# Kernel optimization log

Hardware: AMD Instinct MI355X
Metric: run time of the kernel (lower is better)

Reference implementation:

```python
import jax, jax.numpy as jnp
import numpy as np

SCALE = 4.0  # InputEmbedding scale
D = 16       # coordinate dim (InputEmbedding input_dim)


def _p(k, shape, s=0.05):
    return jax.random.normal(k, shape, dtype=jnp.float32) * s


def setup_inputs() -> dict:
    key = jax.random.key(0)
    ks = jax.random.split(key, 20)
    T, N, E, H = 8, 2048, 256, 768
    return {
        "observed": jax.random.normal(ks[0], (T, N, D), dtype=jnp.float32),
        "emb_W": _p(ks[1], (E, D)), "emb_b": _p(ks[2], (E,)),
        "e1_Wih": _p(ks[3], (3 * H, E)), "e1_Whh": _p(ks[4], (3 * H, H)),
        "e1_bih": _p(ks[5], (3 * H,)), "e1_bhh": _p(ks[6], (3 * H,)),
        "e2_Wih": _p(ks[7], (3 * H, E + H)), "e2_Whh": _p(ks[8], (3 * H, H)),
        "e2_bih": _p(ks[9], (3 * H,)), "e2_bhh": _p(ks[10], (3 * H,)),
        "dec_Wih": _p(ks[11], (3 * H, E)), "dec_Whh": _p(ks[12], (3 * H, H)),
        "dec_bih": _p(ks[13], (3 * H,)), "dec_bhh": _p(ks[14], (3 * H,)),
        "h2n_W": _p(ks[15], (5, H)), "h2n_b": _p(ks[16], (5,)),
        "mix_W": _p(ks[17], (D, 5)), "mix_b": _p(ks[18], (D,)),
        "n_predict": 12,
    }


def _gru(x, h, Wih, Whh, bih, bhh):
    # torch.nn.GRUCell math
    gi = x @ Wih.T + bih          # [N, 3H]
    gh = h @ Whh.T + bhh          # [N, 3H]
    ir, iz, in_ = jnp.split(gi, 3, axis=-1)
    hr, hz, hn = jnp.split(gh, 3, axis=-1)
    r = jax.nn.sigmoid(ir + hr)
    z = jax.nn.sigmoid(iz + hz)
    n = jnp.tanh(in_ + r * hn)
    return (1.0 - z) * n + z * h


def reference(observed, emb_W, emb_b,
              e1_Wih, e1_Whh, e1_bih, e1_bhh,
              e2_Wih, e2_Whh, e2_bih, e2_bhh,
              dec_Wih, dec_Whh, dec_bih, dec_bhh,
              h2n_W, h2n_b, mix_W, mix_b, n_predict):
    T, N, _ = observed.shape
    H = e1_Whh.shape[1]
    embed = lambda v: (SCALE * v) @ emb_W.T + emb_b   # InputEmbedding
    h0 = jnp.zeros((N, H), observed.dtype)

    # --- backward (inverse-time) encoder1 pass ---
    inv = observed[::-1]
    vel_b = inv[:-1] - inv[1:]          # obs2 - obs1 on reversed sequence, [T-1, N, D]
    def step1(h, v):
        return _gru(embed(v), h, e1_Wih, e1_Whh, e1_bih, e1_bhh), None
    h_inv, _ = jax.lax.scan(step1, h0, vel_b)
    # NOTE: original mutates the python hidden_state list in place, so every
    # h_invs entry aliases the FINAL encoder1 state -> h_inv is constant over t.

    # --- forward encoder2 pass (input = [embed(vel), h_inv]) ---
    vel_f = observed[1:] - observed[:-1]   # [T-1, N, D]
    def step2(h, v):
        x = jnp.concatenate([embed(v), h_inv], axis=1)
        return _gru(x, h, e2_Wih, e2_Whh, e2_bih, e2_bhh), None
    h, _ = jax.lax.scan(step2, h0, vel_f)

    def h2n(hs):
        # Hidden2Normal: linear then constrain sigmas / correlation
        n = hs @ h2n_W.T + h2n_b
        return jnp.concatenate(
            [n[:, :2], 0.01 + 0.2 * jax.nn.softplus(n[:, 2:4]), 0.7 * jnp.tanh(n[:, 4:5])],
            axis=1)

    def dec_step(h, obs1, obs2):
        h = _gru(embed(obs2 - obs1), h, dec_Wih, dec_Whh, dec_bih, dec_bhh)
        normal = h2n(h)                                   # [N, 5]
        pos = obs2 + jax.nn.relu(normal @ mix_W.T + mix_b)  # mix: Linear(5 -> 16)
        return h, normal, pos

    # decoder step i=0: (observed[-2], observed[-1]); i=1: (observed[-1], positions[-1].detach())
    h, n0, p0 = dec_step(h, observed[-2], observed[-1])
    h, n1, p1 = dec_step(h, observed[-1], jax.lax.stop_gradient(p0))

    def scan_step(carry, _):
        h, pm2, pm1 = carry
        h, n, p = dec_step(h, jax.lax.stop_gradient(pm2), jax.lax.stop_gradient(pm1))
        return (h, pm1, p), (n, p)
    _, (ns, ps) = jax.lax.scan(scan_step, (h, p0, p1), None, length=n_predict - 2)

    rel_pred_scene = jnp.concatenate([jnp.stack([n0, n1]), ns], axis=0)  # [n_predict, N, 5]
    pred_scene = jnp.concatenate([jnp.stack([p0, p1]), ps], axis=0)      # [n_predict, N, 16]
    return rel_pred_scene, pred_scene
```

## Files before the change

kernel.cpp:

```cpp
#include <hip/hip_runtime.h>
#include <hip/hip_bf16.h>
#include <math.h>

#define H 768
#define NB 2048
#define DD 16

typedef __attribute__((ext_vector_type(8))) short bf16x8;
typedef __attribute__((ext_vector_type(4))) float f32x4;

__device__ __forceinline__ void gload_lds16(const void* g, void* lds) {
  __builtin_amdgcn_global_load_lds((const __attribute__((address_space(1))) void*)g,
                                   (__attribute__((address_space(3))) void*)lds, 16, 0, 0);
}
__device__ __forceinline__ float b2f(short s) {
  union { unsigned int u; float f; } c;
  c.u = ((unsigned int)(unsigned short)s) << 16;
  return c.f;
}
__device__ __forceinline__ short f2bs(float f) {
  __hip_bfloat16 h = __float2bfloat16(f);
  return *(short*)&h;
}

__global__ void k_m1(const float* __restrict__ e1W, const float* __restrict__ e2W,
                     const float* __restrict__ dW, const float* __restrict__ embW,
                     float* __restrict__ M1) {
  int idx = blockIdx.x * 256 + threadIdx.x;
  if (idx >= 3 * 2304 * 16) return;
  int d = idx & 15, g = (idx >> 4) % 2304, s = idx / (2304 * 16);
  const float* W = s == 0 ? e1W : s == 1 ? e2W : dW;
  int ld = s == 1 ? 1024 : 256;
  float sum = 0.f;
  for (int e = 0; e < 256; ++e) sum += W[(size_t)g * ld + e] * embW[e * 16 + d];
  M1[idx] = 4.0f * sum;
}

__global__ void k_biasP(const float* __restrict__ e1W, const float* __restrict__ e2W,
                        const float* __restrict__ dW, const float* __restrict__ embB,
                        const float* b1i, const float* b1h, const float* b2i, const float* b2h,
                        const float* b3i, const float* b3h, float* __restrict__ out) {
  int idx = blockIdx.x * 256 + threadIdx.x;
  if (idx >= 3 * 3072) return;
  int c = idx % 3072, s = idx / 3072;
  int f = (c >> 4) & 3, u = (c >> 6) * 16 + (c & 15);
  const float* W = s == 0 ? e1W : s == 1 ? e2W : dW;
  int ld = s == 1 ? 1024 : 256;
  const float* bi = s == 0 ? b1i : s == 1 ? b2i : b3i;
  const float* bh = s == 0 ? b1h : s == 1 ? b2h : b3h;
  float v;
  if (f == 3) {
    v = bh[1536 + u];
  } else {
    int g = (f < 2 ? f * 768 : 1536) + u;
    float acc = bi[g] + (f < 2 ? bh[g] : 0.f);
    for (int e = 0; e < 256; ++e) acc += W[(size_t)g * ld + e] * embB[e];
    v = acc;
  }
  out[idx] = v;
}

__global__ void k_packB3(const float* __restrict__ W1, const float* __restrict__ W2,
                         const float* __restrict__ W3, const float* __restrict__ M1all,
                         __hip_bfloat16* __restrict__ B1, __hip_bfloat16* __restrict__ B2,
                         __hip_bfloat16* __restrict__ B3) {
  int idx = blockIdx.x * 256 + threadIdx.x;
  if (idx >= 3072 * 800) return;
  int s = blockIdx.y;
  const float* Whh = s == 0 ? W1 : s == 1 ? W2 : W3;
  const float* M1s = M1all + (size_t)s * 2304 * 16;
  __hip_bfloat16* Bp = s == 0 ? B1 : s == 1 ? B2 : B3;
  int k = idx % 800, c = idx / 800;
  int f = (c >> 4) & 3, u = (c >> 6) * 16 + (c & 15);
  float v = 0.f;
  if (k < 768) {
    if (f == 0) v = Whh[(size_t)u * 768 + k];
    else if (f == 1) v = Whh[(size_t)(768 + u) * 768 + k];
    else if (f == 3) v = Whh[(size_t)(1536 + u) * 768 + k];
  } else if (k < 784) {
    if (f < 3) v = M1s[(size_t)(f * 768 + u) * 16 + (k - 768)];
  }
  Bp[idx] = __float2bfloat16(v);
}

__global__ void k_packB2g(const float* __restrict__ e2W, __hip_bfloat16* __restrict__ B2g) {
  int idx = blockIdx.x * 256 + threadIdx.x;
  if (idx >= 3072 * 768) return;
  int k = idx % 768, c = idx / 768;
  int f = (c >> 4) & 3, u = (c >> 6) * 16 + (c & 15);
  float v = (f < 3) ? e2W[(size_t)(f * 768 + u) * 1024 + 256 + k] : 0.f;
  B2g[idx] = __float2bfloat16(v);
}

__global__ void k_vel(const float* __restrict__ obs, __hip_bfloat16* __restrict__ velall) {
  int idx = blockIdx.x * 256 + threadIdx.x;
  if (idx >= 7 * 2048 * 32) return;
  int d = idx & 31, n = (idx >> 5) & 2047, s = idx >> 16;
  float v = 0.f;
  if (d < 16)
    v = obs[((size_t)(s + 1) * NB + n) * DD + d] - obs[((size_t)s * NB + n) * DD + d];
  velall[idx] = __float2bfloat16(v);
}

__global__ __launch_bounds__(256) void k_plain(
    const __hip_bfloat16* __restrict__ A, const __hip_bfloat16* __restrict__ B,
    __hip_bfloat16* __restrict__ C, int ldc) {
  __shared__ __align__(16) __hip_bfloat16 Asm[128 * 32];
  __shared__ __align__(16) __hip_bfloat16 Bsm[128 * 32];
  const int tid = threadIdx.x;
  const int w = tid >> 6, l = tid & 63;
  const int bm = blockIdx.y, bn = blockIdx.x;
  const int wm = w >> 1, wn = w & 1;
  const int lr = l & 15, lk = l >> 4;
  const int ks = (((tid & 3) ^ ((tid >> 3) & 3)) << 3);
  const int lks = ((lk ^ ((lr >> 1) & 3)) << 3);
  f32x4 acc[4][4];
#pragma unroll
  for (int m = 0; m < 4; ++m)
#pragma unroll
    for (int n = 0; n < 4; ++n) acc[m][n] = (f32x4){0.f, 0.f, 0.f, 0.f};
  const int rowA = bm * 128, rowB = bn * 128;
  const int rA = tid >> 2;
  for (int kb = 0; kb < H; kb += 32) {
#pragma unroll
    for (int i = 0; i < 2; ++i) {
      int r = i * 64 + rA;
      gload_lds16(A + (size_t)(rowA + r) * H + kb + ks, (char*)Asm + i * 4096 + w * 1024);
      gload_lds16(B + (size_t)(rowB + r) * H + kb + ks, (char*)Bsm + i * 4096 + w * 1024);
    }
    __syncthreads();
    bf16x8 af[4], bfr[4];
#pragma unroll
    for (int m = 0; m < 4; ++m)
      af[m] = *(const bf16x8*)(Asm + (wm * 64 + m * 16 + lr) * 32 + lks);
#pragma unroll
    for (int n = 0; n < 4; ++n)
      bfr[n] = *(const bf16x8*)(Bsm + (wn * 64 + n * 16 + lr) * 32 + lks);
#pragma unroll
    for (int m = 0; m < 4; ++m)
#pragma unroll
      for (int n = 0; n < 4; ++n)
        acc[m][n] = __builtin_amdgcn_mfma_f32_16x16x32_bf16(af[m], bfr[n], acc[m][n], 0, 0, 0);
    __syncthreads();
  }
#pragma unroll
  for (int m = 0; m < 4; ++m)
#pragma unroll
    for (int n = 0; n < 4; ++n) {
      int col = bn * 128 + wn * 64 + n * 16 + lr;
#pragma unroll
      for (int r4 = 0; r4 < 4; ++r4) {
        int row = rowA + wm * 64 + m * 16 + lk * 4 + r4;
        C[(size_t)row * ldc + col] = __float2bfloat16(acc[m][n][r4]);
      }
    }
}

__global__ __launch_bounds__(256) void k_step(
    const __hip_bfloat16* __restrict__ hin,
    const __hip_bfloat16* __restrict__ vel,
    const __hip_bfloat16* __restrict__ Bp,
    const float* __restrict__ bias,
    const __hip_bfloat16* __restrict__ g2a,
    __hip_bfloat16* __restrict__ hout) {
  __shared__ __align__(16) char lds[49152];
  const int tid = threadIdx.x;
  const int w = tid >> 6, l = tid & 63;
  const int nt = blockIdx.x, bm = blockIdx.y;
  const int rowA = bm * 128, colB = nt * 64;
  const int lr = l & 15, lk = l >> 4;
  const int wbase = w * 1024;
  const int rA = tid >> 2;
  const int ce = (((tid & 3) ^ ((tid >> 3) & 3)) << 3);
  const int lks = ((lk ^ ((lr >> 1) & 3)) << 3);

  auto STAGE = [&](int buf, int kb) {
#pragma unroll
    for (int i_ = 0; i_ < 2; ++i_) {
      int r_ = i_ * 64 + rA;
      const __hip_bfloat16* s_ = (kb < 768)
          ? hin + (size_t)(rowA + r_) * H + kb + ce
          : vel + (size_t)(rowA + r_) * 32 + ce;
      gload_lds16(s_, lds + buf * 12288 + i_ * 4096 + wbase);
    }
    gload_lds16(Bp + (size_t)(colB + rA) * 800 + kb + ce, lds + buf * 12288 + 8192 + wbase);
  };

  f32x4 acc[2][4];
#pragma unroll
  for (int m = 0; m < 2; ++m)
#pragma unroll
    for (int n = 0; n < 4; ++n) acc[m][n] = (f32x4){0.f, 0.f, 0.f, 0.f};

  STAGE(0, 0);
  STAGE(1, 32);
  STAGE(2, 64);

#pragma unroll
  for (int ki = 0; ki < 25; ++ki) {
    if (ki < 23)      asm volatile("s_waitcnt vmcnt(6)" ::: "memory");
    else if (ki == 23) asm volatile("s_waitcnt vmcnt(3)" ::: "memory");
    else               asm volatile("s_waitcnt vmcnt(0)" ::: "memory");
    __builtin_amdgcn_sched_barrier(0);
    __builtin_amdgcn_s_barrier();
    __builtin_amdgcn_sched_barrier(0);
    if (ki < 22) STAGE((ki + 3) & 3, (ki + 3) * 32);
    const char* cur = lds + (ki & 3) * 12288;
    const __hip_bfloat16* Ab = (const __hip_bfloat16*)cur;
    const __hip_bfloat16* Bb = (const __hip_bfloat16*)(cur + 8192);
    bf16x8 a0 = *(const bf16x8*)(Ab + (w * 32 + lr) * 32 + lks);
    bf16x8 a1 = *(const bf16x8*)(Ab + (w * 32 + 16 + lr) * 32 + lks);
    bf16x8 b0 = *(const bf16x8*)(Bb + lr * 32 + lks);
    bf16x8 b1 = *(const bf16x8*)(Bb + (16 + lr) * 32 + lks);
    const bool last = (ki == 24);
    bf16x8 b2 = *(const bf16x8*)(Bb + ((last ? 32 : 48) + lr) * 32 + lks);
    __builtin_amdgcn_s_setprio(1);
    acc[0][0] = __builtin_amdgcn_mfma_f32_16x16x32_bf16(a0, b0, acc[0][0], 0, 0, 0);
    acc[1][0] = __builtin_amdgcn_mfma_f32_16x16x32_bf16(a1, b0, acc[1][0], 0, 0, 0);
    acc[0][1] = __builtin_amdgcn_mfma_f32_16x16x32_bf16(a0, b1, acc[0][1], 0, 0, 0);
    acc[1][1] = __builtin_amdgcn_mfma_f32_16x16x32_bf16(a1, b1, acc[1][1], 0, 0, 0);
    if (last) {
      acc[0][2] = __builtin_amdgcn_mfma_f32_16x16x32_bf16(a0, b2, acc[0][2], 0, 0, 0);
      acc[1][2] = __builtin_amdgcn_mfma_f32_16x16x32_bf16(a1, b2, acc[1][2], 0, 0, 0);
    } else {
      acc[0][3] = __builtin_amdgcn_mfma_f32_16x16x32_bf16(a0, b2, acc[0][3], 0, 0, 0);
      acc[1][3] = __builtin_amdgcn_mfma_f32_16x16x32_bf16(a1, b2, acc[1][3], 0, 0, 0);
    }
    __builtin_amdgcn_s_setprio(0);
  }

  __syncthreads();
  short* T = (short*)lds;
  const float* bp = bias + nt * 64;
#pragma unroll
  for (int n = 0; n < 4; ++n) {
    float bv = bp[n * 16 + lr];
#pragma unroll
    for (int m = 0; m < 2; ++m) {
      int rbase = w * 32 + m * 16 + lk * 4;
#pragma unroll
      for (int r4 = 0; r4 < 4; ++r4)
        T[(rbase + r4) * 72 + n * 16 + lr] = f2bs(acc[m][n][r4] + bv);
    }
  }
  __syncthreads();

  const int row = tid >> 1;
  const int ub = (tid & 1) * 8;
  const size_t grow = (size_t)(rowA + row);
  const short* Tp = T + row * 72;
  bf16x8 Lr = *(const bf16x8*)(Tp + ub);
  bf16x8 Lz = *(const bf16x8*)(Tp + 16 + ub);
  bf16x8 Li = *(const bf16x8*)(Tp + 32 + ub);
  bf16x8 Lh = *(const bf16x8*)(Tp + 48 + ub);
  bf16x8 h8 = *(const bf16x8*)(hin + grow * H + nt * 16 + ub);
  bf16x8 gr, gz, gi_;
  if (g2a) {
    const __hip_bfloat16* gp = g2a + grow * 3072 + nt * 64;
    gr  = *(const bf16x8*)(gp + ub);
    gz  = *(const bf16x8*)(gp + 16 + ub);
    gi_ = *(const bf16x8*)(gp + 32 + ub);
  }
  union { bf16x8 v; short s[8]; } ob;
#pragma unroll
  for (int e = 0; e < 8; ++e) {
    float xr = b2f(Lr[e]), xz = b2f(Lz[e]), xi = b2f(Li[e]), xh = b2f(Lh[e]);
    if (g2a) { xr += b2f(gr[e]); xz += b2f(gz[e]); xi += b2f(gi_[e]); }
    float r = 1.f / (1.f + expf(-xr));
    float z = 1.f / (1.f + expf(-xz));
    float nn = tanhf(xi + r * xh);
    float hv = (1.f - z) * nn + z * b2f(h8[e]);
    ob.s[e] = f2bs(hv);
  }
  *(bf16x8*)(hout + grow * H + nt * 16 + ub) = ob.v;
}

__global__ void k_head(const __hip_bfloat16* __restrict__ h, const float* __restrict__ obs2,
                       const float* __restrict__ h2n_W, const float* __restrict__ h2n_b,
                       const float* __restrict__ mix_W, const float* __restrict__ mix_b,
                       float* __restrict__ rel_out, float* __restrict__ pos_out,
                       __hip_bfloat16* __restrict__ velout) {
  int wv = threadIdx.x >> 6, lane = threadIdx.x & 63;
  int row = blockIdx.x * 4 + wv;
  float s0 = 0.f, s1 = 0.f, s2 = 0.f, s3 = 0.f, s4 = 0.f;
  for (int k = lane; k < H; k += 64) {
    float hv = b2f(((const short*)h)[(size_t)row * H + k]);
    s0 += hv * h2n_W[k];
    s1 += hv * h2n_W[H + k];
    s2 += hv * h2n_W[2 * H + k];
    s3 += hv * h2n_W[3 * H + k];
    s4 += hv * h2n_W[4 * H + k];
  }
#pragma unroll
  for (int off = 32; off; off >>= 1) {
    s0 += __shfl_down(s0, off);
    s1 += __shfl_down(s1, off);
    s2 += __shfl_down(s2, off);
    s3 += __shfl_down(s3, off);
    s4 += __shfl_down(s4, off);
  }
  s0 = __shfl(s0, 0); s1 = __shfl(s1, 0); s2 = __shfl(s2, 0);
  s3 = __shfl(s3, 0); s4 = __shfl(s4, 0);
  float n0 = s0 + h2n_b[0], n1 = s1 + h2n_b[1];
  float x2 = s2 + h2n_b[2], x3 = s3 + h2n_b[3], x4 = s4 + h2n_b[4];
  float n2 = 0.01f + 0.2f * (x2 > 0.f ? x2 + log1pf(expf(-x2)) : log1pf(expf(x2)));
  float n3 = 0.01f + 0.2f * (x3 > 0.f ? x3 + log1pf(expf(-x3)) : log1pf(expf(x3)));
  float n4 = 0.7f * tanhf(x4);
  float rl = 0.f;
  if (lane < DD) {
    float a = mix_b[lane] + n0 * mix_W[lane * 5 + 0] + n1 * mix_W[lane * 5 + 1] +
              n2 * mix_W[lane * 5 + 2] + n3 * mix_W[lane * 5 + 3] + n4 * mix_W[lane * 5 + 4];
    rl = a > 0.f ? a : 0.f;
    pos_out[(size_t)row * DD + lane] = obs2[(size_t)row * DD + lane] + rl;
  }
  if (lane < 32)
    velout[(size_t)row * 32 + lane] = __float2bfloat16(lane < DD ? rl : 0.f);
  if (lane == 0) {
    rel_out[(size_t)row * 5 + 0] = n0;
    rel_out[(size_t)row * 5 + 1] = n1;
    rel_out[(size_t)row * 5 + 2] = n2;
    rel_out[(size_t)row * 5 + 3] = n3;
    rel_out[(size_t)row * 5 + 4] = n4;
  }
}

extern "C" void kernel_launch(void* const* d_in, const int* in_sizes, int n_in,
                              void* d_out, int out_size, void* d_ws, size_t ws_size,
                              hipStream_t stream) {
  (void)in_sizes; (void)n_in; (void)out_size; (void)ws_size;
  const float* observed = (const float*)d_in[0];
  const float* emb_W   = (const float*)d_in[1];
  const float* emb_b   = (const float*)d_in[2];
  const float* e1_Wih  = (const float*)d_in[3];
  const float* e1_Whh  = (const float*)d_in[4];
  const float* e1_bih  = (const float*)d_in[5];
  const float* e1_bhh  = (const float*)d_in[6];
  const float* e2_Wih  = (const float*)d_in[7];
  const float* e2_Whh  = (const float*)d_in[8];
  const float* e2_bih  = (const float*)d_in[9];
  const float* e2_bhh  = (const float*)d_in[10];
  const float* dec_Wih = (const float*)d_in[11];
  const float* dec_Whh = (const float*)d_in[12];
  const float* dec_bih = (const float*)d_in[13];
  const float* dec_bhh = (const float*)d_in[14];
  const float* h2n_W   = (const float*)d_in[15];
  const float* h2n_b   = (const float*)d_in[16];
  const float* mix_W   = (const float*)d_in[17];
  const float* mix_b   = (const float*)d_in[18];

  char* p = (char*)d_ws;
  auto alloc = [&](size_t bytes) { char* r = p; p += (bytes + 255) & ~(size_t)255; return r; };

  __hip_bfloat16* hz     = (__hip_bfloat16*)alloc((size_t)NB * H * 2);
  __hip_bfloat16* hp0    = (__hip_bfloat16*)alloc((size_t)NB * H * 2);
  __hip_bfloat16* hp1    = (__hip_bfloat16*)alloc((size_t)NB * H * 2);
  __hip_bfloat16* velall = (__hip_bfloat16*)alloc((size_t)7 * NB * 32 * 2);
  __hip_bfloat16* dvel   = (__hip_bfloat16*)alloc((size_t)NB * 32 * 2);
  __hip_bfloat16* Bp1    = (__hip_bfloat16*)alloc((size_t)3072 * 800 * 2);
  __hip_bfloat16* Bp2    = (__hip_bfloat16*)alloc((size_t)3072 * 800 * 2);
  __hip_bfloat16* Bp3    = (__hip_bfloat16*)alloc((size_t)3072 * 800 * 2);
  __hip_bfloat16* B2g    = (__hip_bfloat16*)alloc((size_t)3072 * 768 * 2);
  __hip_bfloat16* g2add  = (__hip_bfloat16*)alloc((size_t)NB * 3072 * 2);
  float*          M1     = (float*)alloc((size_t)3 * 2304 * 16 * 4);
  float*          biasP  = (float*)alloc((size_t)3 * 3072 * 4);

  hipMemsetAsync(hz, 0, (size_t)NB * H * 2, stream);
  k_m1<<<(3 * 2304 * 16 + 255) / 256, 256, 0, stream>>>(e1_Wih, e2_Wih, dec_Wih, emb_W, M1);
  k_biasP<<<(3 * 3072 + 255) / 256, 256, 0, stream>>>(e1_Wih, e2_Wih, dec_Wih, emb_b,
                                                      e1_bih, e1_bhh, e2_bih, e2_bhh,
                                                      dec_bih, dec_bhh, biasP);
  k_packB3<<<dim3((3072 * 800 + 255) / 256, 3), 256, 0, stream>>>(e1_Whh, e2_Whh, dec_Whh,
                                                                  M1, Bp1, Bp2, Bp3);
  k_packB2g<<<(3072 * 768 + 255) / 256, 256, 0, stream>>>(e2_Wih, B2g);
  k_vel<<<(7 * NB * 32 + 255) / 256, 256, 0, stream>>>(observed, velall);

  dim3 gs(48, 16);
  const __hip_bfloat16* src;
  __hip_bfloat16* dst = hp0;

  src = hz;
  for (int t = 0; t < 7; ++t) {
    k_step<<<gs, 256, 0, stream>>>(src, velall + (size_t)(6 - t) * NB * 32, Bp1, biasP,
                                   nullptr, dst);
    src = dst;
    dst = (dst == hp0) ? hp1 : hp0;
  }
  k_plain<<<dim3(24, 16), 256, 0, stream>>>(src, B2g, g2add, 3072);

  src = hz;
  for (int t = 0; t < 7; ++t) {
    k_step<<<gs, 256, 0, stream>>>(src, velall + (size_t)t * NB * 32, Bp2, biasP + 3072,
                                   g2add, dst);
    src = dst;
    dst = (dst == hp0) ? hp1 : hp0;
  }

  float* rel  = (float*)d_out;
  float* pred = (float*)d_out + (size_t)12 * NB * 5;
  for (int k = 0; k < 12; ++k) {
    const __hip_bfloat16* vk = (k == 0) ? velall + (size_t)6 * NB * 32 : dvel;
    k_step<<<gs, 256, 0, stream>>>(src, vk, Bp3, biasP + 2 * 3072, nullptr, dst);
    const float* o2 = (k == 0) ? observed + (size_t)7 * NB * DD
                               : pred + (size_t)(k - 1) * NB * DD;
    k_head<<<NB / 4, 256, 0, stream>>>(dst, o2, h2n_W, h2n_b, mix_W, mix_b,
                                       rel + (size_t)k * NB * 5, pred + (size_t)k * NB * DD,
                                       dvel);
    src = dst;
    dst = (dst == hp0) ? hp1 : hp0;
  }
}
```

Before: 773.3 us.

## Halve step-kernel M tile, use 2x2 warp grid, skip zero-state GEMM

The recurrent step kernel moves from 128-row tiles to 64-row tiles and splits its four waves into a 2x2 layout over M and N. The grid doubles to 48x32 and the LDS ring grows to five stages with a four-deep prefetch, with launch bounds asking for more resident blocks. The first step of each encoder, where the hidden state is zero, now runs only the velocity K-slice, which drops the hidden-state GEMM work and the zero-buffer memset. In exchange each block reuses fewer loaded weights, and B tiles are reloaded across twice as many row blocks.

```diff
diff --git a/kernel.cpp b/kernel.cpp
--- a/kernel.cpp
+++ b/kernel.cpp
@@ -7,6 +7,7 @@
 #define DD 16
 
 typedef __attribute__((ext_vector_type(8))) short bf16x8;
+typedef __attribute__((ext_vector_type(4))) short bf16x4;
 typedef __attribute__((ext_vector_type(4))) float f32x4;
 
 __device__ __forceinline__ void gload_lds16(const void* g, void* lds) {
@@ -156,123 +157,126 @@
     }
 }
 
-__global__ __launch_bounds__(256) void k_step(
+__global__ __launch_bounds__(256, 4) void k_step(
     const __hip_bfloat16* __restrict__ hin,
     const __hip_bfloat16* __restrict__ vel,
     const __hip_bfloat16* __restrict__ Bp,
     const float* __restrict__ bias,
     const __hip_bfloat16* __restrict__ g2a,
     __hip_bfloat16* __restrict__ hout) {
-  __shared__ __align__(16) char lds[49152];
+  __shared__ __align__(16) char lds[40960];
   const int tid = threadIdx.x;
   const int w = tid >> 6, l = tid & 63;
   const int nt = blockIdx.x, bm = blockIdx.y;
-  const int rowA = bm * 128, colB = nt * 64;
+  const int rowA = bm * 64, colB = nt * 64;
   const int lr = l & 15, lk = l >> 4;
-  const int wbase = w * 1024;
-  const int rA = tid >> 2;
+  const int wm = w >> 1, wn = w & 1;
+  const int rS = tid >> 2;
   const int ce = (((tid & 3) ^ ((tid >> 3) & 3)) << 3);
   const int lks = ((lk ^ ((lr >> 1) & 3)) << 3);
+  const int wbase = w * 1024;
 
   auto STAGE = [&](int buf, int kb) {
-#pragma unroll
-    for (int i_ = 0; i_ < 2; ++i_) {
-      int r_ = i_ * 64 + rA;
-      const __hip_bfloat16* s_ = (kb < 768)
-          ? hin + (size_t)(rowA + r_) * H + kb + ce
-          : vel + (size_t)(rowA + r_) * 32 + ce;
-      gload_lds16(s_, lds + buf * 12288 + i_ * 4096 + wbase);
+    const __hip_bfloat16* s_ = (kb < 768)
+        ? hin + (size_t)(rowA + rS) * H + kb + ce
+        : vel + (size_t)(rowA + rS) * 32 + ce;
+    gload_lds16(s_, lds + buf * 8192 + wbase);
+    gload_lds16(Bp + (size_t)(colB + rS) * 800 + kb + ce, lds + buf * 8192 + 4096 + wbase);
+  };
+
+  f32x4 acc[2][2];
+#pragma unroll
+  for (int m = 0; m < 2; ++m)
+#pragma unroll
+    for (int n = 0; n < 2; ++n) acc[m][n] = (f32x4){0.f, 0.f, 0.f, 0.f};
+
+  if (hin) {
+    STAGE(0, 0); STAGE(1, 32); STAGE(2, 64); STAGE(3, 96);
+#pragma unroll
+    for (int ki = 0; ki < 25; ++ki) {
+      if (ki < 22)       asm volatile("s_waitcnt vmcnt(6)" ::: "memory");
+      else if (ki == 22) asm volatile("s_waitcnt vmcnt(4)" ::: "memory");
+      else if (ki == 23) asm volatile("s_waitcnt vmcnt(2)" ::: "memory");
+      else               asm volatile("s_waitcnt vmcnt(0)" ::: "memory");
+      __builtin_amdgcn_sched_barrier(0);
+      __builtin_amdgcn_s_barrier();
+      __builtin_amdgcn_sched_barrier(0);
+      if (ki < 21) STAGE((ki + 4) % 5, (ki + 4) * 32);
+      const char* cur = lds + (ki % 5) * 8192;
+      const __hip_bfloat16* Ab = (const __hip_bfloat16*)cur;
+      const __hip_bfloat16* Bb = (const __hip_bfloat16*)(cur + 4096);
+      bf16x8 a0 = *(const bf16x8*)(Ab + (wm * 32 + lr) * 32 + lks);
+      bf16x8 a1 = *(const bf16x8*)(Ab + (wm * 32 + 16 + lr) * 32 + lks);
+      bf16x8 b0 = *(const bf16x8*)(Bb + (wn * 32 + lr) * 32 + lks);
+      bf16x8 b1 = *(const bf16x8*)(Bb + (wn * 32 + 16 + lr) * 32 + lks);
+      __builtin_amdgcn_s_setprio(1);
+      acc[0][0] = __builtin_amdgcn_mfma_f32_16x16x32_bf16(a0, b0, acc[0][0], 0, 0, 0);
+      acc[1][0] = __builtin_amdgcn_mfma_f32_16x16x32_bf16(a1, b0, acc[1][0], 0, 0, 0);
+      acc[0][1] = __builtin_amdgcn_mfma_f32_16x16x32_bf16(a0, b1, acc[0][1], 0, 0, 0);
+      acc[1][1] = __builtin_amdgcn_mfma_f32_16x16x32_bf16(a1, b1, acc[1][1], 0, 0, 0);
+      __builtin_amdgcn_s_setprio(0);
     }
-    gload_lds16(Bp + (size_t)(colB + rA) * 800 + kb + ce, lds + buf * 12288 + 8192 + wbase);
-  };
-
-  f32x4 acc[2][4];
-#pragma unroll
-  for (int m = 0; m < 2; ++m)
-#pragma unroll
-    for (int n = 0; n < 4; ++n) acc[m][n] = (f32x4){0.f, 0.f, 0.f, 0.f};
-
-  STAGE(0, 0);
-  STAGE(1, 32);
-  STAGE(2, 64);
-
-#pragma unroll
-  for (int ki = 0; ki < 25; ++ki) {
-    if (ki < 23)      asm volatile("s_waitcnt vmcnt(6)" ::: "memory");
-    else if (ki == 23) asm volatile("s_waitcnt vmcnt(3)" ::: "memory");
-    else               asm volatile("s_waitcnt vmcnt(0)" ::: "memory");
+  } else {
+    STAGE(0, 768);
+    asm volatile("s_waitcnt vmcnt(0)" ::: "memory");
     __builtin_amdgcn_sched_barrier(0);
     __builtin_amdgcn_s_barrier();
     __builtin_amdgcn_sched_barrier(0);
-    if (ki < 22) STAGE((ki + 3) & 3, (ki + 3) * 32);
-    const char* cur = lds + (ki & 3) * 12288;
-    const __hip_bfloat16* Ab = (const __hip_bfloat16*)cur;
-    const __hip_bfloat16* Bb = (const __hip_bfloat16*)(cur + 8192);
-    bf16x8 a0 = *(const bf16x8*)(Ab + (w * 32 + lr) * 32 + lks);
-    bf16x8 a1 = *(const bf16x8*)(Ab + (w * 32 + 16 + lr) * 32 + lks);
-    bf16x8 b0 = *(const bf16x8*)(Bb + lr * 32 + lks);
-    bf16x8 b1 = *(const bf16x8*)(Bb + (16 + lr) * 32 + lks);
-    const bool last = (ki == 24);
-    bf16x8 b2 = *(const bf16x8*)(Bb + ((last ? 32 : 48) + lr) * 32 + lks);
-    __builtin_amdgcn_s_setprio(1);
+    const __hip_bfloat16* Ab = (const __hip_bfloat16*)lds;
+    const __hip_bfloat16* Bb = (const __hip_bfloat16*)(lds + 4096);
+    bf16x8 a0 = *(const bf16x8*)(Ab + (wm * 32 + lr) * 32 + lks);
+    bf16x8 a1 = *(const bf16x8*)(Ab + (wm * 32 + 16 + lr) * 32 + lks);
+    bf16x8 b0 = *(const bf16x8*)(Bb + (wn * 32 + lr) * 32 + lks);
+    bf16x8 b1 = *(const bf16x8*)(Bb + (wn * 32 + 16 + lr) * 32 + lks);
     acc[0][0] = __builtin_amdgcn_mfma_f32_16x16x32_bf16(a0, b0, acc[0][0], 0, 0, 0);
     acc[1][0] = __builtin_amdgcn_mfma_f32_16x16x32_bf16(a1, b0, acc[1][0], 0, 0, 0);
     acc[0][1] = __builtin_amdgcn_mfma_f32_16x16x32_bf16(a0, b1, acc[0][1], 0, 0, 0);
     acc[1][1] = __builtin_amdgcn_mfma_f32_16x16x32_bf16(a1, b1, acc[1][1], 0, 0, 0);
-    if (last) {
-      acc[0][2] = __builtin_amdgcn_mfma_f32_16x16x32_bf16(a0, b2, acc[0][2], 0, 0, 0);
-      acc[1][2] = __builtin_amdgcn_mfma_f32_16x16x32_bf16(a1, b2, acc[1][2], 0, 0, 0);
-    } else {
-      acc[0][3] = __builtin_amdgcn_mfma_f32_16x16x32_bf16(a0, b2, acc[0][3], 0, 0, 0);
-      acc[1][3] = __builtin_amdgcn_mfma_f32_16x16x32_bf16(a1, b2, acc[1][3], 0, 0, 0);
-    }
-    __builtin_amdgcn_s_setprio(0);
   }
 
   __syncthreads();
   short* T = (short*)lds;
-  const float* bp = bias + nt * 64;
-#pragma unroll
-  for (int n = 0; n < 4; ++n) {
-    float bv = bp[n * 16 + lr];
+#pragma unroll
+  for (int n = 0; n < 2; ++n) {
+    float bv = bias[colB + wn * 32 + n * 16 + lr];
 #pragma unroll
     for (int m = 0; m < 2; ++m) {
-      int rbase = w * 32 + m * 16 + lk * 4;
+      int rbase = wm * 32 + m * 16 + lk * 4;
 #pragma unroll
       for (int r4 = 0; r4 < 4; ++r4)
-        T[(rbase + r4) * 72 + n * 16 + lr] = f2bs(acc[m][n][r4] + bv);
+        T[(rbase + r4) * 72 + wn * 32 + n * 16 + lr] = f2bs(acc[m][n][r4] + bv);
     }
   }
   __syncthreads();
 
-  const int row = tid >> 1;
-  const int ub = (tid & 1) * 8;
+  const int row = tid >> 2, q = tid & 3;
   const size_t grow = (size_t)(rowA + row);
   const short* Tp = T + row * 72;
-  bf16x8 Lr = *(const bf16x8*)(Tp + ub);
-  bf16x8 Lz = *(const bf16x8*)(Tp + 16 + ub);
-  bf16x8 Li = *(const bf16x8*)(Tp + 32 + ub);
-  bf16x8 Lh = *(const bf16x8*)(Tp + 48 + ub);
-  bf16x8 h8 = *(const bf16x8*)(hin + grow * H + nt * 16 + ub);
-  bf16x8 gr, gz, gi_;
+  bf16x4 Lr = *(const bf16x4*)(Tp + q * 4);
+  bf16x4 Lz = *(const bf16x4*)(Tp + 16 + q * 4);
+  bf16x4 Li = *(const bf16x4*)(Tp + 32 + q * 4);
+  bf16x4 Lh = *(const bf16x4*)(Tp + 48 + q * 4);
+  bf16x4 h8 = {};
+  if (hin) h8 = *(const bf16x4*)(hin + grow * H + colB / 4 + q * 4);
+  bf16x4 gr = {}, gz = {}, gi_ = {};
   if (g2a) {
-    const __hip_bfloat16* gp = g2a + grow * 3072 + nt * 64;
-    gr  = *(const bf16x8*)(gp + ub);
-    gz  = *(const bf16x8*)(gp + 16 + ub);
-    gi_ = *(const bf16x8*)(gp + 32 + ub);
-  }
-  union { bf16x8 v; short s[8]; } ob;
-#pragma unroll
-  for (int e = 0; e < 8; ++e) {
+    const __hip_bfloat16* gp = g2a + grow * 3072 + colB;
+    gr  = *(const bf16x4*)(gp + q * 4);
+    gz  = *(const bf16x4*)(gp + 16 + q * 4);
+    gi_ = *(const bf16x4*)(gp + 32 + q * 4);
+  }
+  union { bf16x4 v; short s[4]; } ob;
+#pragma unroll
+  for (int e = 0; e < 4; ++e) {
     float xr = b2f(Lr[e]), xz = b2f(Lz[e]), xi = b2f(Li[e]), xh = b2f(Lh[e]);
     if (g2a) { xr += b2f(gr[e]); xz += b2f(gz[e]); xi += b2f(gi_[e]); }
     float r = 1.f / (1.f + expf(-xr));
     float z = 1.f / (1.f + expf(-xz));
     float nn = tanhf(xi + r * xh);
-    float hv = (1.f - z) * nn + z * b2f(h8[e]);
+    float hv = hin ? ((1.f - z) * nn + z * b2f(h8[e])) : ((1.f - z) * nn);
     ob.s[e] = f2bs(hv);
   }
-  *(bf16x8*)(hout + grow * H + nt * 16 + ub) = ob.v;
+  *(bf16x4*)(hout + grow * H + colB / 4 + q * 4) = ob.v;
 }
 
 __global__ void k_head(const __hip_bfloat16* __restrict__ h, const float* __restrict__ obs2,
@@ -351,7 +355,6 @@
   char* p = (char*)d_ws;
   auto alloc = [&](size_t bytes) { char* r = p; p += (bytes + 255) & ~(size_t)255; return r; };
 
-  __hip_bfloat16* hz     = (__hip_bfloat16*)alloc((size_t)NB * H * 2);
   __hip_bfloat16* hp0    = (__hip_bfloat16*)alloc((size_t)NB * H * 2);
   __hip_bfloat16* hp1    = (__hip_bfloat16*)alloc((size_t)NB * H * 2);
   __hip_bfloat16* velall = (__hip_bfloat16*)alloc((size_t)7 * NB * 32 * 2);
@@ -364,7 +367,6 @@
   float*          M1     = (float*)alloc((size_t)3 * 2304 * 16 * 4);
   float*          biasP  = (float*)alloc((size_t)3 * 3072 * 4);
 
-  hipMemsetAsync(hz, 0, (size_t)NB * H * 2, stream);
   k_m1<<<(3 * 2304 * 16 + 255) / 256, 256, 0, stream>>>(e1_Wih, e2_Wih, dec_Wih, emb_W, M1);
   k_biasP<<<(3 * 3072 + 255) / 256, 256, 0, stream>>>(e1_Wih, e2_Wih, dec_Wih, emb_b,
                                                       e1_bih, e1_bhh, e2_bih, e2_bhh,
@@ -374,22 +376,22 @@
   k_packB2g<<<(3072 * 768 + 255) / 256, 256, 0, stream>>>(e2_Wih, B2g);
   k_vel<<<(7 * NB * 32 + 255) / 256, 256, 0, stream>>>(observed, velall);
 
-  dim3 gs(48, 16);
-  const __hip_bfloat16* src;
+  dim3 gs(48, 32);
+  const __hip_bfloat16* src = nullptr;
   __hip_bfloat16* dst = hp0;
 
-  src = hz;
   for (int t = 0; t < 7; ++t) {
-    k_step<<<gs, 256, 0, stream>>>(src, velall + (size_t)(6 - t) * NB * 32, Bp1, biasP,
+    k_step<<<gs, 256, 0, stream>>>(t == 0 ? nullptr : src,
+                                   velall + (size_t)(6 - t) * NB * 32, Bp1, biasP,
                                    nullptr, dst);
     src = dst;
     dst = (dst == hp0) ? hp1 : hp0;
   }
   k_plain<<<dim3(24, 16), 256, 0, stream>>>(src, B2g, g2add, 3072);
 
-  src = hz;
   for (int t = 0; t < 7; ++t) {
-    k_step<<<gs, 256, 0, stream>>>(src, velall + (size_t)t * NB * 32, Bp2, biasP + 3072,
+    k_step<<<gs, 256, 0, stream>>>(t == 0 ? nullptr : src,
+                                   velall + (size_t)t * NB * 32, Bp2, biasP + 3072,
                                    g2add, dst);
     src = dst;
     dst = (dst == hp0) ? hp1 : hp0;
```

New measurement: 801.9 us. 1.04x slower.
